# Kernel tuning notes

Hardware: AMD Instinct MI355X
Metric: run time of the kernel (lower is better)

The kernel has to match this reference:

```python
import jax, jax.numpy as jnp
import numpy as np

B, S, H, D = 4, 8192, 8, 64  # batch, seq, heads, head_dim
M = 64                        # num random features
EPS = 1e-6


def setup_inputs() -> dict:
    key = jax.random.key(0)
    k1, k2, k3, k4 = jax.random.split(key, 4)
    qs = jax.random.normal(k1, (B, S, H, D), dtype=jnp.float32)
    ks = jax.random.normal(k2, (B, S, H, D), dtype=jnp.float32)
    vs = jax.random.normal(k3, (B, S, H, D), dtype=jnp.float32)
    proj = jax.random.normal(k4, (M, D), dtype=jnp.float32)
    return {"qs": qs, "ks": ks, "vs": vs, "proj": proj}


def _phi(x, proj):
    # stable positive softmax kernel: exp(x @ proj^T - ||x||^2/2) / sqrt(m)
    m = proj.shape[0]
    x_proj = jnp.einsum('...d,md->...m', x, proj)
    h = jnp.sum(jnp.square(x), axis=-1, keepdims=True) * 0.5
    return jnp.exp(x_proj - h) / jnp.sqrt(jnp.asarray(m, x.dtype))


def reference(qs, ks, vs, proj):
    Bq, Q, Hh, Dqk = qs.shape
    K = ks.shape[1]
    Dv = vs.shape[-1]
    # (B, S, H, D) -> (B*H, S, D)
    q = qs.transpose(0, 2, 1, 3).reshape(-1, Q, Dqk)
    k = ks.transpose(0, 2, 1, 3).reshape(-1, K, Dqk)
    v = vs.transpose(0, 2, 1, 3).reshape(-1, K, Dv)
    normalizer = 1.0 / jnp.power(jnp.asarray(Dqk, q.dtype), 0.25)
    q_prime = _phi(q * normalizer, proj)  # (B*H, Q, M)
    k_prime = _phi(k * normalizer, proj)  # (B*H, K, M)
    # fast_attend: linear-time attention
    c = jnp.concatenate([v, jnp.ones((*v.shape[:-1], 1), v.dtype)], axis=-1)  # (B*H, K, Dv+1)
    buf1 = jnp.einsum('bkm,bkc->bmc', k_prime, c)   # (B*H, M, Dv+1)
    buf2 = jnp.einsum('bqm,bmc->bqc', q_prime, buf1)  # (B*H, Q, Dv+1)
    num, den = buf2[..., :-1], buf2[..., -1]
    den = jnp.where(den < EPS, EPS, den)
    ctx = num / den[..., None]
    return ctx.reshape(Bq, Hh, Q, Dv).transpose(0, 2, 1, 3)
```

## Files before the change

kernel.cpp:

```cpp
#include <hip/hip_runtime.h>
#include <hip/hip_bf16.h>

#define S_ 8192
#define H_ 8
#define D_ 64
#define M_ 64
#define BH_ 32
#define CPK_ 80
#define NCHQ 16
#define TILE 64
#define QTILES (S_ / NCHQ / TILE)

typedef short bf16x8 __attribute__((ext_vector_type(8)));
typedef float f32x4 __attribute__((ext_vector_type(4)));

constexpr float XS_ = 0.35355339059327373f * 1.4426950408889634f;
constexpr float HS_ = 0.34657359027997264f;
constexpr float EPS_ = 1e-6f;

__device__ __forceinline__ unsigned short f2bf(float f) {
    unsigned int u = __float_as_uint(f);
    u += 0x7FFFu + ((u >> 16) & 1u);
    return (unsigned short)(u >> 16);
}
__device__ __forceinline__ unsigned int pkbf(float lo, float hi) {
    __hip_bfloat162 t = __float22bfloat162_rn(float2{lo, hi});
    return *reinterpret_cast<unsigned int*>(&t);
}
__device__ __forceinline__ float fexp2(float x) { return __builtin_amdgcn_exp2f(x); }

#define MFMA(a, b, c) __builtin_amdgcn_mfma_f32_16x16x32_bf16((a), (b), (c), 0, 0, 0)
#define SWZ(byteoff, row) ((byteoff) ^ (((row) & 7) << 4))

__global__ void __launch_bounds__(256)
fa_k(const float* __restrict__ ks, const float* __restrict__ vs,
     const float* __restrict__ proj, float* __restrict__ partial,
     int nch, int ktiles)
{
    const int chunk = blockIdx.x;
    const int bh    = blockIdx.y;
    const int b = bh >> 3, h = bh & 7;
    const int tid = threadIdx.x, wid = tid >> 6, lane = tid & 63;
    const int l15 = lane & 15, g = lane >> 4;

    __shared__ __align__(16) char eTb[2][M_ * TILE * 2];
    __shared__ __align__(16) char vTb[2][D_ * TILE * 2];

    const int rows = ktiles * TILE;
    const int s0 = chunk * rows;
    const size_t rs = (size_t)H_ * D_;
    const float* kb = ks + ((size_t)b * S_ * H_ + h) * D_;
    const float* vb = vs + ((size_t)b * S_ * H_ + h) * D_;

    bf16x8 pf[4][2];
#pragma unroll
    for (int mt = 0; mt < 4; ++mt)
#pragma unroll
        for (int kk = 0; kk < 2; ++kk) {
            const float* p = proj + (mt * 16 + l15) * D_ + kk * 32 + g * 8;
            float4 a = *(const float4*)p, c = *(const float4*)(p + 4);
            union { bf16x8 v; unsigned int u[4]; } F;
            F.u[0] = pkbf(a.x, a.y); F.u[1] = pkbf(a.z, a.w);
            F.u[2] = pkbf(c.x, c.y); F.u[3] = pkbf(c.z, c.w);
            pf[mt][kk] = F.v;
        }

    bf16x8 onef = {0, 0, 0, 0, 0, 0, 0, 0};
    if (l15 == 0) {
#pragma unroll
        for (int j = 0; j < 8; ++j) onef[j] = (short)0x3F80;
    }

    f32x4 acc[5];
#pragma unroll
    for (int ci = 0; ci < 5; ++ci) acc[ci] = (f32x4){0.f, 0.f, 0.f, 0.f};

    auto loadT = [&](int t, float4* kp, float4* vp) {
        int sb = s0 + t * TILE;
        const float* krow = kb + (size_t)(sb + wid * 16 + l15) * rs;
        kp[0] = *(const float4*)(krow + g * 8);
        kp[1] = *(const float4*)(krow + g * 8 + 4);
        kp[2] = *(const float4*)(krow + 32 + g * 8);
        kp[3] = *(const float4*)(krow + 32 + g * 8 + 4);
        const float* vrow = vb + (size_t)(sb + wid * 16 + l15) * rs;
        vp[0] = *(const float4*)(vrow + g * 8);
        vp[1] = *(const float4*)(vrow + g * 8 + 4);
        vp[2] = *(const float4*)(vrow + 32 + g * 8);
        vp[3] = *(const float4*)(vrow + 32 + g * 8 + 4);
    };

    auto body = [&](int t, int p, const float4* kc, const float4* vc,
                    float4* kn, float4* vn) {
        if (t + 1 < ktiles) loadT(t + 1, kn, vn);

        float kx[16];
#pragma unroll
        for (int i = 0; i < 4; ++i) {
            kx[4 * i + 0] = kc[i].x * XS_; kx[4 * i + 1] = kc[i].y * XS_;
            kx[4 * i + 2] = kc[i].z * XS_; kx[4 * i + 3] = kc[i].w * XS_;
        }
        float sq = 0.f;
#pragma unroll
        for (int j = 0; j < 16; ++j) sq += kx[j] * kx[j];
        sq += __shfl_xor(sq, 16);
        sq += __shfl_xor(sq, 32);
        float hrow = sq * HS_ + 3.0f;

        union { bf16x8 v; unsigned int u[4]; } A0, A1;
#pragma unroll
        for (int i = 0; i < 4; ++i) {
            A0.u[i] = pkbf(kx[2 * i], kx[2 * i + 1]);
            A1.u[i] = pkbf(kx[8 + 2 * i], kx[9 + 2 * i]);
        }

        f32x4 pa[4];
#pragma unroll
        for (int mt = 0; mt < 4; ++mt) {
            pa[mt] = (f32x4){0.f, 0.f, 0.f, 0.f};
            pa[mt] = MFMA(A0.v, pf[mt][0], pa[mt]);
            pa[mt] = MFMA(A1.v, pf[mt][1], pa[mt]);
        }

        float hr[4];
#pragma unroll
        for (int r = 0; r < 4; ++r) hr[r] = __shfl(hrow, 4 * g + r);

        char* etp = eTb[p];
        char* vtp = vTb[p];
#pragma unroll
        for (int mt = 0; mt < 4; ++mt) {
            float e0 = fexp2(pa[mt][0] - hr[0]);
            float e1 = fexp2(pa[mt][1] - hr[1]);
            float e2 = fexp2(pa[mt][2] - hr[2]);
            float e3 = fexp2(pa[mt][3] - hr[3]);
            unsigned long long pk = (unsigned long long)pkbf(e0, e1)
                                  | ((unsigned long long)pkbf(e2, e3) << 32);
            int m = mt * 16 + l15;
            *(unsigned long long*)(etp + SWZ(m * 128 + 32 * wid + 8 * g, m)) = pk;
        }
        {
            int row = wid * 16 + l15;
            float vv[16];
#pragma unroll
            for (int i = 0; i < 4; ++i) {
                vv[4 * i + 0] = vc[i].x; vv[4 * i + 1] = vc[i].y;
                vv[4 * i + 2] = vc[i].z; vv[4 * i + 3] = vc[i].w;
            }
#pragma unroll
            for (int q = 0; q < 4; ++q) {
                int c0 = g * 8 + 2 * q;
                unsigned int pA = pkbf(vv[2 * q], vv[2 * q + 1]);
                *(unsigned short*)(vtp + SWZ(c0 * 128 + 2 * row, c0)) =
                    (unsigned short)pA;
                *(unsigned short*)(vtp + SWZ((c0 + 1) * 128 + 2 * row, c0 + 1)) =
                    (unsigned short)(pA >> 16);
                int c1 = 32 + c0;
                unsigned int pB = pkbf(vv[8 + 2 * q], vv[9 + 2 * q]);
                *(unsigned short*)(vtp + SWZ(c1 * 128 + 2 * row, c1)) =
                    (unsigned short)pB;
                *(unsigned short*)(vtp + SWZ((c1 + 1) * 128 + 2 * row, c1 + 1)) =
                    (unsigned short)(pB >> 16);
            }
        }
        __syncthreads();

        bf16x8 a2[2];
        {
            int m = wid * 16 + l15;
            a2[0] = *(const bf16x8*)(etp + SWZ(m * 128 + 16 * g, m));
            a2[1] = *(const bf16x8*)(etp + SWZ(m * 128 + 16 * g + 64, m));
        }
#pragma unroll
        for (int ci = 0; ci < 4; ++ci) {
            int c = ci * 16 + l15;
            bf16x8 b0 = *(const bf16x8*)(vtp + SWZ(c * 128 + 16 * g, c));
            bf16x8 b1 = *(const bf16x8*)(vtp + SWZ(c * 128 + 16 * g + 64, c));
            acc[ci] = MFMA(a2[0], b0, acc[ci]);
            acc[ci] = MFMA(a2[1], b1, acc[ci]);
        }
        acc[4] = MFMA(a2[0], onef, acc[4]);
        acc[4] = MFMA(a2[1], onef, acc[4]);
    };

    float4 ka[4], kb2[4];
    float4 va[4], vb2[4];
    loadT(0, ka, va);
    for (int t = 0; t + 2 <= ktiles; t += 2) {
        body(t, 0, ka, va, kb2, vb2);
        body(t + 1, 1, kb2, vb2, ka, va);
    }

    float* dst = partial + ((size_t)bh * nch + chunk) * (M_ * CPK_);
#pragma unroll
    for (int ci = 0; ci < 5; ++ci)
#pragma unroll
        for (int r = 0; r < 4; ++r)
            dst[(wid * 16 + 4 * g + r) * CPK_ + ci * 16 + l15] = acc[ci][r];
}

__global__ void __launch_bounds__(256)
fa_r(const float* __restrict__ partial, float* __restrict__ buf1, int nch)
{
    int e = blockIdx.x * 256 + threadIdx.x;
    if (e >= BH_ * M_ * CPK_) return;
    int bh = e / (M_ * CPK_);
    int r  = e - bh * (M_ * CPK_);
    const float* src = partial + (size_t)bh * nch * (M_ * CPK_) + r;
    float s0 = 0.f, s1 = 0.f, s2 = 0.f, s3 = 0.f;
    int ch = 0;
    for (; ch + 4 <= nch; ch += 4) {
        s0 += src[(size_t)(ch + 0) * (M_ * CPK_)];
        s1 += src[(size_t)(ch + 1) * (M_ * CPK_)];
        s2 += src[(size_t)(ch + 2) * (M_ * CPK_)];
        s3 += src[(size_t)(ch + 3) * (M_ * CPK_)];
    }
    for (; ch < nch; ++ch) s0 += src[(size_t)ch * (M_ * CPK_)];
    buf1[e] = (s0 + s1) + (s2 + s3);
}

__global__ void __launch_bounds__(256)
fa_q(const float* __restrict__ qs, const float* __restrict__ proj,
     const float* __restrict__ buf1, float* __restrict__ out)
{
    const int chunk = blockIdx.x;
    const int bh    = blockIdx.y;
    const int b = bh >> 3, h = bh & 7;
    const int tid = threadIdx.x, wid = tid >> 6, lane = tid & 63;
    const int l15 = lane & 15, g = lane >> 4;

    __shared__ __align__(16) char eLb[2][TILE * M_ * 2];
    __shared__ __align__(16) char b1tb[CPK_ * M_ * 2];

    const int rows = S_ / NCHQ;
    const int s0 = chunk * rows;
    const size_t rs = (size_t)H_ * D_;
    const float* qb = qs + ((size_t)b * S_ * H_ + h) * D_;

    const float* b1 = buf1 + (size_t)bh * (M_ * CPK_);
    for (int i = tid; i < M_ * CPK_; i += 256) {
        int m = i / CPK_, c = i - m * CPK_;
        *(unsigned short*)(b1tb + SWZ(c * 128 + 2 * m, c)) = f2bf(b1[i]);
    }

    bf16x8 pf[4][2];
#pragma unroll
    for (int mt = 0; mt < 4; ++mt)
#pragma unroll
        for (int kk = 0; kk < 2; ++kk) {
            const float* p = proj + (mt * 16 + l15) * D_ + kk * 32 + g * 8;
            float4 a = *(const float4*)p, c = *(const float4*)(p + 4);
            union { bf16x8 v; unsigned int u[4]; } F;
            F.u[0] = pkbf(a.x, a.y); F.u[1] = pkbf(a.z, a.w);
            F.u[2] = pkbf(c.x, c.y); F.u[3] = pkbf(c.z, c.w);
            pf[mt][kk] = F.v;
        }
    __syncthreads();

    bf16x8 af3[5][2];
#pragma unroll
    for (int ci = 0; ci < 5; ++ci)
#pragma unroll
        for (int kk = 0; kk < 2; ++kk) {
            int c = ci * 16 + l15;
            af3[ci][kk] = *(const bf16x8*)(b1tb + SWZ(c * 128 + 16 * g + 64 * kk, c));
        }

    auto loadQ = [&](int t, float4* qp) {
        int sb = s0 + t * TILE;
        const float* qrow = qb + (size_t)(sb + wid * 16 + l15) * rs;
        qp[0] = *(const float4*)(qrow + g * 8);
        qp[1] = *(const float4*)(qrow + g * 8 + 4);
        qp[2] = *(const float4*)(qrow + 32 + g * 8);
        qp[3] = *(const float4*)(qrow + 32 + g * 8 + 4);
    };

    auto body = [&](int t, int p, const float4* qc, float4* qn) {
        if (t + 1 < QTILES) loadQ(t + 1, qn);

        float kx[16];
#pragma unroll
        for (int i = 0; i < 4; ++i) {
            kx[4 * i + 0] = qc[i].x * XS_; kx[4 * i + 1] = qc[i].y * XS_;
            kx[4 * i + 2] = qc[i].z * XS_; kx[4 * i + 3] = qc[i].w * XS_;
        }
        float sq = 0.f;
#pragma unroll
        for (int j = 0; j < 16; ++j) sq += kx[j] * kx[j];
        sq += __shfl_xor(sq, 16);
        sq += __shfl_xor(sq, 32);
        float hrow = sq * HS_ + 3.0f;

        union { bf16x8 v; unsigned int u[4]; } A0, A1;
#pragma unroll
        for (int i = 0; i < 4; ++i) {
            A0.u[i] = pkbf(kx[2 * i], kx[2 * i + 1]);
            A1.u[i] = pkbf(kx[8 + 2 * i], kx[9 + 2 * i]);
        }

        f32x4 pa[4];
#pragma unroll
        for (int mt = 0; mt < 4; ++mt) {
            pa[mt] = (f32x4){0.f, 0.f, 0.f, 0.f};
            pa[mt] = MFMA(A0.v, pf[mt][0], pa[mt]);
            pa[mt] = MFMA(A1.v, pf[mt][1], pa[mt]);
        }

        float hr[4];
#pragma unroll
        for (int r = 0; r < 4; ++r) hr[r] = __shfl(hrow, 4 * g + r);

        char* elp = eLb[p];
#pragma unroll
        for (int mt = 0; mt < 4; ++mt) {
            int m = mt * 16 + l15;
            float e0 = fexp2(pa[mt][0] - hr[0]);
            float e1 = fexp2(pa[mt][1] - hr[1]);
            float e2 = fexp2(pa[mt][2] - hr[2]);
            float e3 = fexp2(pa[mt][3] - hr[3]);
            unsigned int p01 = pkbf(e0, e1), p23 = pkbf(e2, e3);
            int q0 = wid * 16 + 4 * g;
            *(unsigned short*)(elp + SWZ((q0 + 0) * 128 + 2 * m, q0 + 0)) =
                (unsigned short)p01;
            *(unsigned short*)(elp + SWZ((q0 + 1) * 128 + 2 * m, q0 + 1)) =
                (unsigned short)(p01 >> 16);
            *(unsigned short*)(elp + SWZ((q0 + 2) * 128 + 2 * m, q0 + 2)) =
                (unsigned short)p23;
            *(unsigned short*)(elp + SWZ((q0 + 3) * 128 + 2 * m, q0 + 3)) =
                (unsigned short)(p23 >> 16);
        }
        __syncthreads();

        bf16x8 b3[2];
        {
            int qrow = wid * 16 + l15;
            b3[0] = *(const bf16x8*)(elp + SWZ(qrow * 128 + 16 * g, qrow));
            b3[1] = *(const bf16x8*)(elp + SWZ(qrow * 128 + 16 * g + 64, qrow));
        }
        f32x4 dt[5];
#pragma unroll
        for (int ci = 0; ci < 5; ++ci) {
            dt[ci] = (f32x4){0.f, 0.f, 0.f, 0.f};
            dt[ci] = MFMA(af3[ci][0], b3[0], dt[ci]);
            dt[ci] = MFMA(af3[ci][1], b3[1], dt[ci]);
        }

        float den = __shfl(dt[4][0], l15);
        float rd = 1.0f / fmaxf(den, EPS_);

        int sg = s0 + t * TILE + wid * 16 + l15;
        size_t base = (((size_t)b * S_ + sg) * H_ + h) * D_;
#pragma unroll
        for (int ci = 0; ci < 4; ++ci) {
            f32x4 o;
#pragma unroll
            for (int r = 0; r < 4; ++r) o[r] = dt[ci][r] * rd;
            *(f32x4*)(out + base + ci * 16 + 4 * g) = o;
        }
    };

    float4 qa[4], qb2[4];
    loadQ(0, qa);
    for (int t = 0; t < QTILES; t += 2) {
        body(t, 0, qa, qb2);
        body(t + 1, 1, qb2, qa);
    }
}

extern "C" void kernel_launch(void* const* d_in, const int* in_sizes, int n_in,
                              void* d_out, int out_size, void* d_ws, size_t ws_size,
                              hipStream_t stream)
{
    const float* qs   = (const float*)d_in[0];
    const float* ks   = (const float*)d_in[1];
    const float* vs   = (const float*)d_in[2];
    const float* proj = (const float*)d_in[3];
    float* out = (float*)d_out;

    int nch = 16;
    while (nch > 8 &&
           (size_t)BH_ * (size_t)(nch + 1) * (M_ * CPK_) * sizeof(float) > ws_size)
        nch >>= 1;
    int ktiles = S_ / nch / TILE;

    float* partial = (float*)d_ws;
    float* buf1 = partial + (size_t)BH_ * nch * (M_ * CPK_);

    fa_k<<<dim3(nch, BH_), 256, 0, stream>>>(ks, vs, proj, partial, nch, ktiles);
    int nred = (BH_ * M_ * CPK_ + 255) / 256;
    fa_r<<<dim3(nred), 256, 0, stream>>>(partial, buf1, nch);
    fa_q<<<dim3(NCHQ, BH_), 256, 0, stream>>>(qs, proj, buf1, out);
}
```

Before: 72.79 us.

## Make fa_k warps independent with per-warp V staging and end-of-block reduction

Restructures the K/V pass so each warp handles its own 32 rows per step. Exp features stay in registers as the MFMA A operand, and only V goes through a per-warp double-buffered LDS slot, so the per-tile __syncthreads is gone. Each warp accumulates a full 64x80 partial in registers, and these are summed through shared memory with a serialized reduction at the end. The cost is far more accumulator registers (launch bounds now ask for 2 blocks per CU), a fixed 16-chunk split with no check against workspace size, and a serialized cross-warp reduction.

```diff
diff --git a/kernel.cpp b/kernel.cpp
--- a/kernel.cpp
+++ b/kernel.cpp
@@ -7,6 +7,8 @@
 #define M_ 64
 #define BH_ 32
 #define CPK_ 80
+#define NCH_ 16
+#define ITERS_ 4
 #define NCHQ 16
 #define TILE 64
 #define QTILES (S_ / NCHQ / TILE)
@@ -32,10 +34,9 @@
 #define MFMA(a, b, c) __builtin_amdgcn_mfma_f32_16x16x32_bf16((a), (b), (c), 0, 0, 0)
 #define SWZ(byteoff, row) ((byteoff) ^ (((row) & 7) << 4))
 
-__global__ void __launch_bounds__(256)
+__global__ void __launch_bounds__(256, 2)
 fa_k(const float* __restrict__ ks, const float* __restrict__ vs,
-     const float* __restrict__ proj, float* __restrict__ partial,
-     int nch, int ktiles)
+     const float* __restrict__ proj, float* __restrict__ partial)
 {
     const int chunk = blockIdx.x;
     const int bh    = blockIdx.y;
@@ -43,14 +44,13 @@
     const int tid = threadIdx.x, wid = tid >> 6, lane = tid & 63;
     const int l15 = lane & 15, g = lane >> 4;
 
-    __shared__ __align__(16) char eTb[2][M_ * TILE * 2];
-    __shared__ __align__(16) char vTb[2][D_ * TILE * 2];
-
-    const int rows = ktiles * TILE;
-    const int s0 = chunk * rows;
+    __shared__ __align__(16) char vW[4][2][64 * 64];
+    __shared__ float red[M_ * CPK_];
+
     const size_t rs = (size_t)H_ * D_;
     const float* kb = ks + ((size_t)b * S_ * H_ + h) * D_;
     const float* vb = vs + ((size_t)b * S_ * H_ + h) * D_;
+    const int rbase = chunk * (ITERS_ * 128) + wid * 32;
 
     bf16x8 pf[4][2];
 #pragma unroll
@@ -71,131 +71,157 @@
         for (int j = 0; j < 8; ++j) onef[j] = (short)0x3F80;
     }
 
-    f32x4 acc[5];
-#pragma unroll
-    for (int ci = 0; ci < 5; ++ci) acc[ci] = (f32x4){0.f, 0.f, 0.f, 0.f};
-
-    auto loadT = [&](int t, float4* kp, float4* vp) {
-        int sb = s0 + t * TILE;
-        const float* krow = kb + (size_t)(sb + wid * 16 + l15) * rs;
-        kp[0] = *(const float4*)(krow + g * 8);
-        kp[1] = *(const float4*)(krow + g * 8 + 4);
-        kp[2] = *(const float4*)(krow + 32 + g * 8);
-        kp[3] = *(const float4*)(krow + 32 + g * 8 + 4);
-        const float* vrow = vb + (size_t)(sb + wid * 16 + l15) * rs;
-        vp[0] = *(const float4*)(vrow + g * 8);
-        vp[1] = *(const float4*)(vrow + g * 8 + 4);
-        vp[2] = *(const float4*)(vrow + 32 + g * 8);
-        vp[3] = *(const float4*)(vrow + 32 + g * 8 + 4);
+    f32x4 acc[4][5];
+#pragma unroll
+    for (int mt = 0; mt < 4; ++mt)
+#pragma unroll
+        for (int ci = 0; ci < 5; ++ci) acc[mt][ci] = (f32x4){0.f, 0.f, 0.f, 0.f};
+
+    auto loadX = [&](const float* xb, int t, float4* xp) {
+        const float* r0 = xb + (size_t)(rbase + t * 128 + l15) * rs;
+        xp[0] = *(const float4*)(r0 + g * 8);
+        xp[1] = *(const float4*)(r0 + g * 8 + 4);
+        xp[2] = *(const float4*)(r0 + 32 + g * 8);
+        xp[3] = *(const float4*)(r0 + 32 + g * 8 + 4);
+        const float* r1 = r0 + 16 * rs;
+        xp[4] = *(const float4*)(r1 + g * 8);
+        xp[5] = *(const float4*)(r1 + g * 8 + 4);
+        xp[6] = *(const float4*)(r1 + 32 + g * 8);
+        xp[7] = *(const float4*)(r1 + 32 + g * 8 + 4);
     };
 
-    auto body = [&](int t, int p, const float4* kc, const float4* vc,
-                    float4* kn, float4* vn) {
-        if (t + 1 < ktiles) loadT(t + 1, kn, vn);
-
-        float kx[16];
-#pragma unroll
-        for (int i = 0; i < 4; ++i) {
-            kx[4 * i + 0] = kc[i].x * XS_; kx[4 * i + 1] = kc[i].y * XS_;
-            kx[4 * i + 2] = kc[i].z * XS_; kx[4 * i + 3] = kc[i].w * XS_;
-        }
-        float sq = 0.f;
-#pragma unroll
-        for (int j = 0; j < 16; ++j) sq += kx[j] * kx[j];
-        sq += __shfl_xor(sq, 16);
-        sq += __shfl_xor(sq, 32);
-        float hrow = sq * HS_ + 3.0f;
-
-        union { bf16x8 v; unsigned int u[4]; } A0, A1;
-#pragma unroll
-        for (int i = 0; i < 4; ++i) {
-            A0.u[i] = pkbf(kx[2 * i], kx[2 * i + 1]);
-            A1.u[i] = pkbf(kx[8 + 2 * i], kx[9 + 2 * i]);
-        }
-
-        f32x4 pa[4];
-#pragma unroll
-        for (int mt = 0; mt < 4; ++mt) {
-            pa[mt] = (f32x4){0.f, 0.f, 0.f, 0.f};
-            pa[mt] = MFMA(A0.v, pf[mt][0], pa[mt]);
-            pa[mt] = MFMA(A1.v, pf[mt][1], pa[mt]);
-        }
-
-        float hr[4];
-#pragma unroll
-        for (int r = 0; r < 4; ++r) hr[r] = __shfl(hrow, 4 * g + r);
-
-        char* etp = eTb[p];
-        char* vtp = vTb[p];
-#pragma unroll
-        for (int mt = 0; mt < 4; ++mt) {
-            float e0 = fexp2(pa[mt][0] - hr[0]);
-            float e1 = fexp2(pa[mt][1] - hr[1]);
-            float e2 = fexp2(pa[mt][2] - hr[2]);
-            float e3 = fexp2(pa[mt][3] - hr[3]);
-            unsigned long long pk = (unsigned long long)pkbf(e0, e1)
-                                  | ((unsigned long long)pkbf(e2, e3) << 32);
-            int m = mt * 16 + l15;
-            *(unsigned long long*)(etp + SWZ(m * 128 + 32 * wid + 8 * g, m)) = pk;
-        }
-        {
-            int row = wid * 16 + l15;
+    auto storeV = [&](const float4* vp, int buf) {
+        char* base = (char*)vW + wid * 8192 + buf * 4096;
+        int id0 = ((l15 >> 2) & 3) * 8 + (l15 & 3);
+#pragma unroll
+        for (int s = 0; s < 2; ++s) {
+            int id = id0 + 4 * s;
             float vv[16];
 #pragma unroll
             for (int i = 0; i < 4; ++i) {
-                vv[4 * i + 0] = vc[i].x; vv[4 * i + 1] = vc[i].y;
-                vv[4 * i + 2] = vc[i].z; vv[4 * i + 3] = vc[i].w;
+                float4 q = vp[4 * s + i];
+                vv[4 * i + 0] = q.x; vv[4 * i + 1] = q.y;
+                vv[4 * i + 2] = q.z; vv[4 * i + 3] = q.w;
             }
 #pragma unroll
-            for (int q = 0; q < 4; ++q) {
-                int c0 = g * 8 + 2 * q;
-                unsigned int pA = pkbf(vv[2 * q], vv[2 * q + 1]);
-                *(unsigned short*)(vtp + SWZ(c0 * 128 + 2 * row, c0)) =
+            for (int p2 = 0; p2 < 4; ++p2) {
+                int cA = g * 8 + 2 * p2;
+                unsigned int pA = pkbf(vv[2 * p2], vv[2 * p2 + 1]);
+                *(unsigned short*)(base + cA * 64 + ((2 * id) ^ ((cA & 3) << 4))) =
                     (unsigned short)pA;
-                *(unsigned short*)(vtp + SWZ((c0 + 1) * 128 + 2 * row, c0 + 1)) =
+                int cB = cA + 1;
+                *(unsigned short*)(base + cB * 64 + ((2 * id) ^ ((cB & 3) << 4))) =
                     (unsigned short)(pA >> 16);
-                int c1 = 32 + c0;
-                unsigned int pB = pkbf(vv[8 + 2 * q], vv[9 + 2 * q]);
-                *(unsigned short*)(vtp + SWZ(c1 * 128 + 2 * row, c1)) =
+                int cC = 32 + cA;
+                unsigned int pB = pkbf(vv[8 + 2 * p2], vv[9 + 2 * p2]);
+                *(unsigned short*)(base + cC * 64 + ((2 * id) ^ ((cC & 3) << 4))) =
                     (unsigned short)pB;
-                *(unsigned short*)(vtp + SWZ((c1 + 1) * 128 + 2 * row, c1 + 1)) =
+                int cD = cC + 1;
+                *(unsigned short*)(base + cD * 64 + ((2 * id) ^ ((cD & 3) << 4))) =
                     (unsigned short)(pB >> 16);
             }
         }
+    };
+
+    auto body = [&](int t, const float4* kc, float4* kn, float4* vn) {
+        if (t + 1 < ITERS_) { loadX(kb, t + 1, kn); loadX(vb, t + 1, vn); }
+
+        float kx0[16], kx1[16];
+#pragma unroll
+        for (int i = 0; i < 4; ++i) {
+            kx0[4*i+0] = kc[i].x * XS_; kx0[4*i+1] = kc[i].y * XS_;
+            kx0[4*i+2] = kc[i].z * XS_; kx0[4*i+3] = kc[i].w * XS_;
+            kx1[4*i+0] = kc[4+i].x * XS_; kx1[4*i+1] = kc[4+i].y * XS_;
+            kx1[4*i+2] = kc[4+i].z * XS_; kx1[4*i+3] = kc[4+i].w * XS_;
+        }
+        float sq0 = 0.f, sq1 = 0.f;
+#pragma unroll
+        for (int j = 0; j < 16; ++j) { sq0 += kx0[j]*kx0[j]; sq1 += kx1[j]*kx1[j]; }
+        sq0 += __shfl_xor(sq0, 16); sq0 += __shfl_xor(sq0, 32);
+        sq1 += __shfl_xor(sq1, 16); sq1 += __shfl_xor(sq1, 32);
+        float h0 = sq0 * HS_ + 3.0f, h1 = sq1 * HS_ + 3.0f;
+
+        union { bf16x8 v; unsigned int u[4]; } A00, A01, A10, A11;
+#pragma unroll
+        for (int i = 0; i < 4; ++i) {
+            A00.u[i] = pkbf(kx0[2*i], kx0[2*i+1]);
+            A01.u[i] = pkbf(kx0[8+2*i], kx0[9+2*i]);
+            A10.u[i] = pkbf(kx1[2*i], kx1[2*i+1]);
+            A11.u[i] = pkbf(kx1[8+2*i], kx1[9+2*i]);
+        }
+
+        f32x4 pa0[4], pa1[4];
+#pragma unroll
+        for (int mt = 0; mt < 4; ++mt) {
+            pa0[mt] = (f32x4){0.f, 0.f, 0.f, 0.f};
+            pa0[mt] = MFMA(A00.v, pf[mt][0], pa0[mt]);
+            pa0[mt] = MFMA(A01.v, pf[mt][1], pa0[mt]);
+            pa1[mt] = (f32x4){0.f, 0.f, 0.f, 0.f};
+            pa1[mt] = MFMA(A10.v, pf[mt][0], pa1[mt]);
+            pa1[mt] = MFMA(A11.v, pf[mt][1], pa1[mt]);
+        }
+
+        float hr0[4], hr1[4];
+#pragma unroll
+        for (int r = 0; r < 4; ++r) {
+            hr0[r] = __shfl(h0, 4 * g + r);
+            hr1[r] = __shfl(h1, 4 * g + r);
+        }
+
+        bf16x8 eA[4];
+#pragma unroll
+        for (int mt = 0; mt < 4; ++mt) {
+            union { bf16x8 v; unsigned int u[4]; } E;
+            E.u[0] = pkbf(fexp2(pa0[mt][0]-hr0[0]), fexp2(pa0[mt][1]-hr0[1]));
+            E.u[1] = pkbf(fexp2(pa0[mt][2]-hr0[2]), fexp2(pa0[mt][3]-hr0[3]));
+            E.u[2] = pkbf(fexp2(pa1[mt][0]-hr1[0]), fexp2(pa1[mt][1]-hr1[1]));
+            E.u[3] = pkbf(fexp2(pa1[mt][2]-hr1[2]), fexp2(pa1[mt][3]-hr1[3]));
+            eA[mt] = E.v;
+        }
+
+        const char* rb2 = (const char*)vW + wid * 8192 + (t & 1) * 4096;
+        bf16x8 vB[4];
+#pragma unroll
+        for (int ct = 0; ct < 4; ++ct) {
+            int c = ct * 16 + l15;
+            vB[ct] = *(const bf16x8*)(rb2 + c * 64 + ((16 * g) ^ ((c & 3) << 4)));
+        }
+#pragma unroll
+        for (int mt = 0; mt < 4; ++mt) {
+#pragma unroll
+            for (int ct = 0; ct < 4; ++ct)
+                acc[mt][ct] = MFMA(eA[mt], vB[ct], acc[mt][ct]);
+            acc[mt][4] = MFMA(eA[mt], onef, acc[mt][4]);
+        }
+
+        if (t + 1 < ITERS_) storeV(vn, (t + 1) & 1);
+    };
+
+    float4 k0[8], k1[8], v0[8], v1[8];
+    loadX(kb, 0, k0);
+    loadX(vb, 0, v0);
+    storeV(v0, 0);
+    body(0, k0, k1, v1);
+    body(1, k1, k0, v0);
+    body(2, k0, k1, v1);
+    body(3, k1, k0, v0);
+
+    for (int i = tid; i < M_ * CPK_; i += 256) red[i] = 0.f;
+    __syncthreads();
+    for (int w = 0; w < 4; ++w) {
+        if (wid == w) {
+#pragma unroll
+            for (int mt = 0; mt < 4; ++mt)
+#pragma unroll
+                for (int ct = 0; ct < 5; ++ct)
+#pragma unroll
+                    for (int r = 0; r < 4; ++r)
+                        red[(mt*16 + 4*g + r) * CPK_ + ct*16 + l15] += acc[mt][ct][r];
+        }
         __syncthreads();
-
-        bf16x8 a2[2];
-        {
-            int m = wid * 16 + l15;
-            a2[0] = *(const bf16x8*)(etp + SWZ(m * 128 + 16 * g, m));
-            a2[1] = *(const bf16x8*)(etp + SWZ(m * 128 + 16 * g + 64, m));
-        }
-#pragma unroll
-        for (int ci = 0; ci < 4; ++ci) {
-            int c = ci * 16 + l15;
-            bf16x8 b0 = *(const bf16x8*)(vtp + SWZ(c * 128 + 16 * g, c));
-            bf16x8 b1 = *(const bf16x8*)(vtp + SWZ(c * 128 + 16 * g + 64, c));
-            acc[ci] = MFMA(a2[0], b0, acc[ci]);
-            acc[ci] = MFMA(a2[1], b1, acc[ci]);
-        }
-        acc[4] = MFMA(a2[0], onef, acc[4]);
-        acc[4] = MFMA(a2[1], onef, acc[4]);
-    };
-
-    float4 ka[4], kb2[4];
-    float4 va[4], vb2[4];
-    loadT(0, ka, va);
-    for (int t = 0; t + 2 <= ktiles; t += 2) {
-        body(t, 0, ka, va, kb2, vb2);
-        body(t + 1, 1, kb2, vb2, ka, va);
     }
-
-    float* dst = partial + ((size_t)bh * nch + chunk) * (M_ * CPK_);
-#pragma unroll
-    for (int ci = 0; ci < 5; ++ci)
-#pragma unroll
-        for (int r = 0; r < 4; ++r)
-            dst[(wid * 16 + 4 * g + r) * CPK_ + ci * 16 + l15] = acc[ci][r];
+    float* dst = partial + ((size_t)bh * NCH_ + chunk) * (M_ * CPK_);
+    for (int i = tid; i < M_ * CPK_; i += 256) dst[i] = red[i];
 }
 
 __global__ void __launch_bounds__(256)
@@ -376,17 +402,11 @@
     const float* proj = (const float*)d_in[3];
     float* out = (float*)d_out;
 
-    int nch = 16;
-    while (nch > 8 &&
-           (size_t)BH_ * (size_t)(nch + 1) * (M_ * CPK_) * sizeof(float) > ws_size)
-        nch >>= 1;
-    int ktiles = S_ / nch / TILE;
-
     float* partial = (float*)d_ws;
-    float* buf1 = partial + (size_t)BH_ * nch * (M_ * CPK_);
-
-    fa_k<<<dim3(nch, BH_), 256, 0, stream>>>(ks, vs, proj, partial, nch, ktiles);
+    float* buf1 = partial + (size_t)BH_ * NCH_ * (M_ * CPK_);
+
+    fa_k<<<dim3(NCH_, BH_), 256, 0, stream>>>(ks, vs, proj, partial);
     int nred = (BH_ * M_ * CPK_ + 255) / 256;
-    fa_r<<<dim3(nred), 256, 0, stream>>>(partial, buf1, nch);
+    fa_r<<<dim3(nred), 256, 0, stream>>>(partial, buf1, NCH_);
     fa_q<<<dim3(NCHQ, BH_), 256, 0, stream>>>(qs, proj, buf1, out);
 }
```

Measured after the change: 74.45 us. 1.02x slower.
